# Performance work log

Measured on AMD Instinct MI355X. Metric: run time of the kernel, lower is better.

## Reference

```python
import jax, jax.numpy as jnp
import numpy as np

BN_EPS = 1e-5
TAU = 1.0  # gumbel temperature

def setup_inputs() -> dict:
    key = jax.random.key(0)
    ks = jax.random.split(key, 6)
    B, O, F, H, HID = 32, 4096, 256, 8, 128
    x = jax.random.normal(ks[0], (B, O, F), dtype=jnp.float32)
    gumbel_noise = jax.random.gumbel(ks[1], (B, O, H), dtype=jnp.float32)
    W_in = jax.random.normal(ks[2], (F, HID), dtype=jnp.float32) * (1.0 / np.sqrt(F))
    b_in = jnp.zeros((HID,), jnp.float32)
    W_blk = jax.random.normal(ks[3], (HID, HID), dtype=jnp.float32) * (1.0 / np.sqrt(HID))
    b_blk = jnp.zeros((HID,), jnp.float32)
    bn_gamma = jnp.ones((HID,), jnp.float32)
    bn_beta = jnp.zeros((HID,), jnp.float32)
    W_fc = jax.random.normal(ks[4], (HID, H), dtype=jnp.float32) * (1.0 / np.sqrt(HID))
    b_fc = jnp.zeros((H,), jnp.float32)
    return {"x": x, "gumbel_noise": gumbel_noise, "W_in": W_in, "b_in": b_in,
            "W_blk": W_blk, "b_blk": b_blk, "bn_gamma": bn_gamma, "bn_beta": bn_beta,
            "W_fc": W_fc, "b_fc": b_fc}

def reference(x, gumbel_noise, W_in, b_in, W_blk, b_blk, bn_gamma, bn_beta, W_fc, b_fc):
    B, O, F = x.shape
    xf = x.reshape(B * O, F)
    # DynamicNetwork head: input linear + relu, one residual block (Linear+BN+ReLU), fc
    h = jax.nn.relu(xf @ W_in + b_in)  # (B*O, HID)
    z = h @ W_blk + b_blk
    mu = z.mean(axis=0)
    var = z.var(axis=0)  # biased var, matches BatchNorm training normalization
    z = (z - mu) * jax.lax.rsqrt(var + BN_EPS) * bn_gamma + bn_beta
    h = jax.nn.relu(z) + h  # residual
    logits = (h @ W_fc + b_fc).reshape(B, O, -1)  # (B, O, H)
    # mask out zero-norm observations
    mask = (jnp.linalg.norm(x, axis=2) != 0)[..., None].astype(x.dtype)  # (B, O, 1)
    logits = logits * mask
    # gumbel softmax over observation dim (soft)
    w = jax.nn.softmax((logits + gumbel_noise) / TAU, axis=1)  # (B, O, H)
    # weighted sum pooling: algebraically the repeat-multiply-sum in the original
    pooled = jnp.einsum('boh,bof->bhf', w, x)  # (B, H, F)
    return pooled.reshape(B, -1)  # (B, H*F)
```

## Files before the change

kernel.cpp:

```cpp
#include <hip/hip_runtime.h>
#include <hip/hip_bf16.h>
#include <math.h>

#define MB_ 131072
#define F_  256
#define HID_ 128
#define H_  8
#define O_  4096
#define B_  32

typedef __attribute__((ext_vector_type(8))) short short8;
typedef __attribute__((ext_vector_type(4))) float f32x4;

static __device__ __forceinline__ unsigned short f2bf(float f) {
    unsigned int u = __float_as_uint(f);
    unsigned int r = (u + 0x7fffu + ((u >> 16) & 1u)) >> 16;
    return (unsigned short)r;
}
static __device__ __forceinline__ float bf2f(unsigned short u) {
    return __uint_as_float(((unsigned int)u) << 16);
}
static __device__ __forceinline__ float bflo(unsigned int u) {
    return __uint_as_float(u << 16);
}
static __device__ __forceinline__ float bfhi(unsigned int u) {
    return __uint_as_float(u & 0xffff0000u);
}

__global__ __launch_bounds__(256) void k_prep(
    const float* __restrict__ W_in, const float* __restrict__ W_blk,
    unsigned short* __restrict__ WinT, unsigned short* __restrict__ WblkT)
{
    const int idx = blockIdx.x * 256 + threadIdx.x;
    if (idx < 32768) {
        const int n = idx >> 8, k = idx & 255;
        WinT[idx] = f2bf(W_in[(size_t)k * HID_ + n]);
    } else {
        const int i2 = idx - 32768;
        const int n = i2 >> 7, k = i2 & 127;
        WblkT[i2] = f2bf(W_blk[(size_t)k * HID_ + n]);
    }
}

__global__ __launch_bounds__(256) void k_mfma_in(
    const float* __restrict__ x, const unsigned short* __restrict__ WinT,
    const float* __restrict__ b_in,
    unsigned short* __restrict__ h_out, float* __restrict__ mask_out)
{
    __shared__ unsigned short a_s[128 * 40];
    __shared__ unsigned short b_s[128 * 40];
    __shared__ float msum_s[128];
    const int tid = threadIdx.x;
    const int R0 = blockIdx.x * 128;
    const int lp_r = tid >> 3;
    const int lp_c = tid & 7;
    const int wave = tid >> 6;
    const int wrow = wave >> 1, wcol = wave & 1;
    const int lane = tid & 63;
    const int lm = lane & 15, quad = lane >> 4;

    if (tid < 128) msum_s[tid] = 0.f;
    float ms[4] = {0.f, 0.f, 0.f, 0.f};

    f32x4 acc[4][4];
#pragma unroll
    for (int i = 0; i < 4; i++)
#pragma unroll
        for (int j = 0; j < 4; j++) acc[i][j] = (f32x4){0.f, 0.f, 0.f, 0.f};

    for (int kt = 0; kt < 8; kt++) {
#pragma unroll
        for (int p = 0; p < 4; p++) {
            const int r = lp_r + 32 * p;
            const float4 v = *(const float4*)(x + (size_t)(R0 + r) * F_ + kt * 32 + lp_c * 4);
            ms[p] += v.x * v.x + v.y * v.y + v.z * v.z + v.w * v.w;
            ushort4 o;
            o.x = f2bf(v.x); o.y = f2bf(v.y); o.z = f2bf(v.z); o.w = f2bf(v.w);
            *(ushort4*)(&a_s[r * 40 + lp_c * 4]) = o;
        }
#pragma unroll
        for (int p = 0; p < 4; p++) {
            const int n = lp_r + 32 * p;
            const ushort4 wv = *(const ushort4*)(WinT + (size_t)n * F_ + kt * 32 + lp_c * 4);
            *(ushort4*)(&b_s[n * 40 + lp_c * 4]) = wv;
        }
        __syncthreads();
        short8 af[4], bfr[4];
#pragma unroll
        for (int mi = 0; mi < 4; mi++)
            af[mi] = *(const short8*)(&a_s[(wrow * 64 + mi * 16 + lm) * 40 + quad * 8]);
#pragma unroll
        for (int ni = 0; ni < 4; ni++)
            bfr[ni] = *(const short8*)(&b_s[(wcol * 64 + ni * 16 + lm) * 40 + quad * 8]);
#pragma unroll
        for (int mi = 0; mi < 4; mi++)
#pragma unroll
            for (int ni = 0; ni < 4; ni++)
                acc[mi][ni] = __builtin_amdgcn_mfma_f32_16x16x32_bf16(af[mi], bfr[ni], acc[mi][ni], 0, 0, 0);
        __syncthreads();
    }

#pragma unroll
    for (int p = 0; p < 4; p++) atomicAdd(&msum_s[lp_r + 32 * p], ms[p]);

    float bcol[4];
#pragma unroll
    for (int ni = 0; ni < 4; ni++) bcol[ni] = b_in[wcol * 64 + ni * 16 + lm];
#pragma unroll
    for (int mi = 0; mi < 4; mi++)
#pragma unroll
        for (int r = 0; r < 4; r++) {
            const size_t row = (size_t)R0 + wrow * 64 + mi * 16 + quad * 4 + r;
#pragma unroll
            for (int ni = 0; ni < 4; ni++) {
                const float v = fmaxf(acc[mi][ni][r] + bcol[ni], 0.f);
                h_out[row * HID_ + wcol * 64 + ni * 16 + lm] = f2bf(v);
            }
        }
    __syncthreads();
    if (tid < 128) mask_out[R0 + tid] = (msum_s[tid] != 0.f) ? 1.f : 0.f;
}

__global__ __launch_bounds__(256) void k_mfma_blk(
    const unsigned short* __restrict__ h_in, const unsigned short* __restrict__ WblkT,
    const float* __restrict__ b_blk, unsigned short* __restrict__ z_out,
    float* __restrict__ sumP, float* __restrict__ sumsqP)
{
    __shared__ unsigned short a_s[128 * 40];
    __shared__ unsigned short b_s[128 * 40];
    __shared__ float csum_s[128], csumsq_s[128];
    const int tid = threadIdx.x;
    const int R0 = blockIdx.x * 128;
    const int lp_r = tid >> 3;
    const int lp_c = tid & 7;
    const int wave = tid >> 6;
    const int wrow = wave >> 1, wcol = wave & 1;
    const int lane = tid & 63;
    const int lm = lane & 15, quad = lane >> 4;

    if (tid < 128) { csum_s[tid] = 0.f; csumsq_s[tid] = 0.f; }

    f32x4 acc[4][4];
#pragma unroll
    for (int i = 0; i < 4; i++)
#pragma unroll
        for (int j = 0; j < 4; j++) acc[i][j] = (f32x4){0.f, 0.f, 0.f, 0.f};

    for (int kt = 0; kt < 4; kt++) {
#pragma unroll
        for (int p = 0; p < 4; p++) {
            const int r = lp_r + 32 * p;
            const ushort4 v = *(const ushort4*)(h_in + (size_t)(R0 + r) * HID_ + kt * 32 + lp_c * 4);
            *(ushort4*)(&a_s[r * 40 + lp_c * 4]) = v;
        }
#pragma unroll
        for (int p = 0; p < 4; p++) {
            const int n = lp_r + 32 * p;
            const ushort4 wv = *(const ushort4*)(WblkT + (size_t)n * HID_ + kt * 32 + lp_c * 4);
            *(ushort4*)(&b_s[n * 40 + lp_c * 4]) = wv;
        }
        __syncthreads();
        short8 af[4], bfr[4];
#pragma unroll
        for (int mi = 0; mi < 4; mi++)
            af[mi] = *(const short8*)(&a_s[(wrow * 64 + mi * 16 + lm) * 40 + quad * 8]);
#pragma unroll
        for (int ni = 0; ni < 4; ni++)
            bfr[ni] = *(const short8*)(&b_s[(wcol * 64 + ni * 16 + lm) * 40 + quad * 8]);
#pragma unroll
        for (int mi = 0; mi < 4; mi++)
#pragma unroll
            for (int ni = 0; ni < 4; ni++)
                acc[mi][ni] = __builtin_amdgcn_mfma_f32_16x16x32_bf16(af[mi], bfr[ni], acc[mi][ni], 0, 0, 0);
        __syncthreads();
    }

    float bcol[4];
#pragma unroll
    for (int ni = 0; ni < 4; ni++) bcol[ni] = b_blk[wcol * 64 + ni * 16 + lm];
    float s_c[4] = {0.f, 0.f, 0.f, 0.f}, ss_c[4] = {0.f, 0.f, 0.f, 0.f};
#pragma unroll
    for (int mi = 0; mi < 4; mi++)
#pragma unroll
        for (int r = 0; r < 4; r++) {
            const size_t row = (size_t)R0 + wrow * 64 + mi * 16 + quad * 4 + r;
#pragma unroll
            for (int ni = 0; ni < 4; ni++) {
                const float zv = acc[mi][ni][r] + bcol[ni];
                s_c[ni] += zv;
                ss_c[ni] += zv * zv;
                z_out[row * HID_ + wcol * 64 + ni * 16 + lm] = f2bf(zv);
            }
        }
#pragma unroll
    for (int ni = 0; ni < 4; ni++) {
        atomicAdd(&csum_s[wcol * 64 + ni * 16 + lm], s_c[ni]);
        atomicAdd(&csumsq_s[wcol * 64 + ni * 16 + lm], ss_c[ni]);
    }
    __syncthreads();
    if (tid < 128) {
        sumP[(size_t)blockIdx.x * 128 + tid] = csum_s[tid];
        sumsqP[(size_t)blockIdx.x * 128 + tid] = csumsq_s[tid];
    }
}

__global__ __launch_bounds__(256) void k_bnfin(
    const float* __restrict__ sumP, const float* __restrict__ sumsqP,
    const float* __restrict__ gamma, const float* __restrict__ beta,
    float* __restrict__ scale, float* __restrict__ shift)
{
    const int c = blockIdx.x;
    const int tid = threadIdx.x;
    float s = 0.f, ss = 0.f;
    for (int i = tid; i < 1024; i += 256) {
        s  += sumP[(size_t)i * 128 + c];
        ss += sumsqP[(size_t)i * 128 + c];
    }
#pragma unroll
    for (int off = 32; off; off >>= 1) {
        s  += __shfl_xor(s, off, 64);
        ss += __shfl_xor(ss, off, 64);
    }
    __shared__ float rs[4], rss[4];
    const int wid = tid >> 6, lane = tid & 63;
    if (lane == 0) { rs[wid] = s; rss[wid] = ss; }
    __syncthreads();
    if (tid == 0) {
        const float S  = rs[0] + rs[1] + rs[2] + rs[3];
        const float SS = rss[0] + rss[1] + rss[2] + rss[3];
        const float inv_m = 1.0f / (float)MB_;
        const float mu = S * inv_m;
        const float var = SS * inv_m - mu * mu;
        const float sc = gamma[c] * rsqrtf(var + 1e-5f);
        scale[c] = sc;
        shift[c] = beta[c] - mu * sc;
    }
}

__global__ __launch_bounds__(256) void k_logits(
    const unsigned short* __restrict__ h_in, const unsigned short* __restrict__ z_in,
    const float* __restrict__ scale, const float* __restrict__ shift,
    const float* __restrict__ W_fc, const float* __restrict__ b_fc,
    const float* __restrict__ mask, const float* __restrict__ gumbel,
    float* __restrict__ t_out)
{
    __shared__ float wfc_s[128 * 8];
    __shared__ float sc_s[128], sh_s[128];
    const int tid = threadIdx.x;
    for (int i = tid; i < 1024; i += 256) wfc_s[i] = W_fc[i];
    if (tid < 128) { sc_s[tid] = scale[tid]; sh_s[tid] = shift[tid]; }
    __syncthreads();

    const size_t row = (size_t)blockIdx.x * 256 + tid;
    float acc[8];
#pragma unroll
    for (int j = 0; j < 8; j++) acc[j] = 0.f;

    const uint4* hp = (const uint4*)(h_in + row * HID_);
    const uint4* zp = (const uint4*)(z_in + row * HID_);
#pragma unroll 2
    for (int kc = 0; kc < 16; kc++) {
        const uint4 hq = hp[kc];
        const uint4 zq = zp[kc];
        unsigned int hs[4] = {hq.x, hq.y, hq.z, hq.w};
        unsigned int zs[4] = {zq.x, zq.y, zq.z, zq.w};
#pragma unroll
        for (int p = 0; p < 4; p++) {
            const int k = kc * 8 + p * 2;
            const float hf0 = bflo(hs[p]), hf1 = bfhi(hs[p]);
            const float zf0 = bflo(zs[p]), zf1 = bfhi(zs[p]);
            const float hb0 = fmaxf(zf0 * sc_s[k] + sh_s[k], 0.f) + hf0;
            const float hb1 = fmaxf(zf1 * sc_s[k + 1] + sh_s[k + 1], 0.f) + hf1;
#pragma unroll
            for (int j = 0; j < 8; j++)
                acc[j] += hb0 * wfc_s[k * 8 + j] + hb1 * wfc_s[(k + 1) * 8 + j];
        }
    }
    const float mk = mask[row];
    const float4 g0 = *(const float4*)(gumbel + row * 8);
    const float4 g1 = *(const float4*)(gumbel + row * 8 + 4);
    float4 t0, t1;
    t0.x = (acc[0] + b_fc[0]) * mk + g0.x;
    t0.y = (acc[1] + b_fc[1]) * mk + g0.y;
    t0.z = (acc[2] + b_fc[2]) * mk + g0.z;
    t0.w = (acc[3] + b_fc[3]) * mk + g0.w;
    t1.x = (acc[4] + b_fc[4]) * mk + g1.x;
    t1.y = (acc[5] + b_fc[5]) * mk + g1.y;
    t1.z = (acc[6] + b_fc[6]) * mk + g1.z;
    t1.w = (acc[7] + b_fc[7]) * mk + g1.w;
    *(float4*)(t_out + row * 8) = t0;
    *(float4*)(t_out + row * 8 + 4) = t1;
}

__global__ __launch_bounds__(256) void k_softmax(
    const float* __restrict__ t_in, float* __restrict__ w_out)
{
    const int bh = blockIdx.x;
    const int b = bh >> 3, hh = bh & 7;
    const int tid = threadIdx.x;
    const float* tp = t_in + (size_t)b * O_ * H_ + hh;
    float v[16];
    float mx = -3.4e38f;
#pragma unroll
    for (int it = 0; it < 16; it++) {
        v[it] = tp[(size_t)(it * 256 + tid) * 8];
        mx = fmaxf(mx, v[it]);
    }
#pragma unroll
    for (int off = 32; off; off >>= 1) mx = fmaxf(mx, __shfl_xor(mx, off, 64));
    __shared__ float rm[4];
    __shared__ float rsum[4];
    const int wid = tid >> 6, lane = tid & 63;
    if (lane == 0) rm[wid] = mx;
    __syncthreads();
    mx = fmaxf(fmaxf(rm[0], rm[1]), fmaxf(rm[2], rm[3]));
    float sum = 0.f;
#pragma unroll
    for (int it = 0; it < 16; it++) { v[it] = __expf(v[it] - mx); sum += v[it]; }
#pragma unroll
    for (int off = 32; off; off >>= 1) sum += __shfl_xor(sum, off, 64);
    if (lane == 0) rsum[wid] = sum;
    __syncthreads();
    sum = rsum[0] + rsum[1] + rsum[2] + rsum[3];
    const float inv = 1.f / sum;
    float* wp = w_out + (size_t)bh * O_;
#pragma unroll
    for (int it = 0; it < 16; it++) wp[it * 256 + tid] = v[it] * inv;
}

__global__ __launch_bounds__(256) void k_pool(
    const float* __restrict__ x, const float* __restrict__ w_in,
    float* __restrict__ pp)
{
    __shared__ float ws_s[8][256];
    const int tid = threadIdx.x;
    const int oc = blockIdx.x;
    const int b = blockIdx.y;
#pragma unroll
    for (int hh = 0; hh < 8; hh++)
        ws_s[hh][tid] = w_in[((size_t)(b * 8 + hh)) * O_ + oc * 256 + tid];
    __syncthreads();
    float acc[8];
#pragma unroll
    for (int hh = 0; hh < 8; hh++) acc[hh] = 0.f;
    const float* xp = x + ((size_t)b * O_ + oc * 256) * F_ + tid;
    for (int o = 0; o < 256; o++) {
        const float xv = xp[(size_t)o * F_];
#pragma unroll
        for (int hh = 0; hh < 8; hh++) acc[hh] += ws_s[hh][o] * xv;
    }
    float* outp = pp + ((size_t)oc * 32 + b) * 2048;
#pragma unroll
    for (int hh = 0; hh < 8; hh++) outp[hh * 256 + tid] = acc[hh];
}

__global__ __launch_bounds__(256) void k_reduce_pool(
    const float* __restrict__ pp, float* __restrict__ out)
{
    const size_t i = (size_t)blockIdx.x * 256 + threadIdx.x;
    float s = 0.f;
#pragma unroll
    for (int oc = 0; oc < 16; oc++) s += pp[(size_t)oc * 65536 + i];
    out[i] = s;
}

extern "C" void kernel_launch(void* const* d_in, const int* in_sizes, int n_in,
                              void* d_out, int out_size, void* d_ws, size_t ws_size,
                              hipStream_t stream)
{
    const float* x      = (const float*)d_in[0];
    const float* gumbel = (const float*)d_in[1];
    const float* W_in   = (const float*)d_in[2];
    const float* b_in   = (const float*)d_in[3];
    const float* W_blk  = (const float*)d_in[4];
    const float* b_blk  = (const float*)d_in[5];
    const float* gamma  = (const float*)d_in[6];
    const float* beta   = (const float*)d_in[7];
    const float* W_fc   = (const float*)d_in[8];
    const float* b_fc   = (const float*)d_in[9];
    float* out = (float*)d_out;
    char* ws = (char*)d_ws;

    unsigned short* h_bf  = (unsigned short*)(ws + 0);
    unsigned short* z_bf  = (unsigned short*)(ws + 33554432);
    float* mask   = (float*)(ws + 67108864);
    float* sumP   = (float*)(ws + 67633152);
    float* sumsqP = (float*)(ws + 68157440);
    float* scale  = (float*)(ws + 68681728);
    float* shift  = (float*)(ws + 68682240);
    float* t_buf  = (float*)(ws + 68682752);
    float* w_buf  = (float*)(ws + 72877056);
    float* pp     = (float*)(ws + 77071360);
    unsigned short* WinT  = (unsigned short*)(ws + 81265664);
    unsigned short* WblkT = (unsigned short*)(ws + 81331200);

    k_prep<<<192, 256, 0, stream>>>(W_in, W_blk, WinT, WblkT);
    k_mfma_in<<<1024, 256, 0, stream>>>(x, WinT, b_in, h_bf, mask);
    k_mfma_blk<<<1024, 256, 0, stream>>>(h_bf, WblkT, b_blk, z_bf, sumP, sumsqP);
    k_bnfin<<<128, 256, 0, stream>>>(sumP, sumsqP, gamma, beta, scale, shift);
    k_logits<<<512, 256, 0, stream>>>(h_bf, z_bf, scale, shift, W_fc, b_fc, mask, gumbel, t_buf);
    k_softmax<<<256, 256, 0, stream>>>(t_buf, w_buf);
    k_pool<<<dim3(16, 32), 256, 0, stream>>>(x, w_buf, pp);
    k_reduce_pool<<<256, 256, 0, stream>>>(pp, out);
}
```

Baseline: 303.5 us.

## Fuse both GEMMs into phase A, recompute z in logits kernel, transpose logits layout

The input GEMM and the block GEMM are merged into one kernel. h stays in shared memory and only BN statistics are produced, so z is never written to memory. The logits kernel recomputes z with MFMA from h instead of reading a stored z, then applies BN, the residual and fc, and writes logits in (b,h,o) layout so softmax can use contiguous float4 loads. The pooling kernel is split into twice as many O-chunks. This trades extra recompute of the second GEMM and a larger partial reduction for removing the 32MB z round trip.

```diff
diff --git a/kernel.cpp b/kernel.cpp
--- a/kernel.cpp
+++ b/kernel.cpp
@@ -19,12 +19,6 @@
 }
 static __device__ __forceinline__ float bf2f(unsigned short u) {
     return __uint_as_float(((unsigned int)u) << 16);
-}
-static __device__ __forceinline__ float bflo(unsigned int u) {
-    return __uint_as_float(u << 16);
-}
-static __device__ __forceinline__ float bfhi(unsigned int u) {
-    return __uint_as_float(u & 0xffff0000u);
 }
 
 __global__ __launch_bounds__(256) void k_prep(
@@ -42,14 +36,19 @@
     }
 }
 
-__global__ __launch_bounds__(256) void k_mfma_in(
+__global__ __launch_bounds__(256) void k_phaseA(
     const float* __restrict__ x, const unsigned short* __restrict__ WinT,
-    const float* __restrict__ b_in,
-    unsigned short* __restrict__ h_out, float* __restrict__ mask_out)
+    const unsigned short* __restrict__ WblkT,
+    const float* __restrict__ b_in, const float* __restrict__ b_blk,
+    unsigned short* __restrict__ h_out, float* __restrict__ mask_out,
+    float* __restrict__ sumP, float* __restrict__ sumsqP)
 {
     __shared__ unsigned short a_s[128 * 40];
     __shared__ unsigned short b_s[128 * 40];
+    __shared__ unsigned short hb_s[128 * 136];
     __shared__ float msum_s[128];
+    __shared__ float csum_s[128], csumsq_s[128];
+
     const int tid = threadIdx.x;
     const int R0 = blockIdx.x * 128;
     const int lp_r = tid >> 3;
@@ -59,7 +58,7 @@
     const int lane = tid & 63;
     const int lm = lane & 15, quad = lane >> 4;
 
-    if (tid < 128) msum_s[tid] = 0.f;
+    if (tid < 128) { msum_s[tid] = 0.f; csum_s[tid] = 0.f; csumsq_s[tid] = 0.f; }
     float ms[4] = {0.f, 0.f, 0.f, 0.f};
 
     f32x4 acc[4][4];
@@ -102,57 +101,39 @@
 
 #pragma unroll
     for (int p = 0; p < 4; p++) atomicAdd(&msum_s[lp_r + 32 * p], ms[p]);
-
-    float bcol[4];
-#pragma unroll
-    for (int ni = 0; ni < 4; ni++) bcol[ni] = b_in[wcol * 64 + ni * 16 + lm];
-#pragma unroll
-    for (int mi = 0; mi < 4; mi++)
-#pragma unroll
-        for (int r = 0; r < 4; r++) {
-            const size_t row = (size_t)R0 + wrow * 64 + mi * 16 + quad * 4 + r;
-#pragma unroll
-            for (int ni = 0; ni < 4; ni++) {
-                const float v = fmaxf(acc[mi][ni][r] + bcol[ni], 0.f);
-                h_out[row * HID_ + wcol * 64 + ni * 16 + lm] = f2bf(v);
+    {
+        float bcol[4];
+#pragma unroll
+        for (int ni = 0; ni < 4; ni++) bcol[ni] = b_in[wcol * 64 + ni * 16 + lm];
+#pragma unroll
+        for (int mi = 0; mi < 4; mi++)
+#pragma unroll
+            for (int r = 0; r < 4; r++) {
+                const int row = wrow * 64 + mi * 16 + quad * 4 + r;
+#pragma unroll
+                for (int ni = 0; ni < 4; ni++) {
+                    const int col = wcol * 64 + ni * 16 + lm;
+                    hb_s[row * 136 + col] = f2bf(fmaxf(acc[mi][ni][r] + bcol[ni], 0.f));
+                }
             }
-        }
-    __syncthreads();
+    }
+    __syncthreads();
+
+    {
+        const int row = tid >> 1, half = tid & 1;
+#pragma unroll
+        for (int c8 = 0; c8 < 8; c8++) {
+            const short8 v = *(const short8*)(&hb_s[row * 136 + half * 64 + c8 * 8]);
+            *(short8*)(h_out + (size_t)(R0 + row) * HID_ + half * 64 + c8 * 8) = v;
+        }
+    }
     if (tid < 128) mask_out[R0 + tid] = (msum_s[tid] != 0.f) ? 1.f : 0.f;
-}
-
-__global__ __launch_bounds__(256) void k_mfma_blk(
-    const unsigned short* __restrict__ h_in, const unsigned short* __restrict__ WblkT,
-    const float* __restrict__ b_blk, unsigned short* __restrict__ z_out,
-    float* __restrict__ sumP, float* __restrict__ sumsqP)
-{
-    __shared__ unsigned short a_s[128 * 40];
-    __shared__ unsigned short b_s[128 * 40];
-    __shared__ float csum_s[128], csumsq_s[128];
-    const int tid = threadIdx.x;
-    const int R0 = blockIdx.x * 128;
-    const int lp_r = tid >> 3;
-    const int lp_c = tid & 7;
-    const int wave = tid >> 6;
-    const int wrow = wave >> 1, wcol = wave & 1;
-    const int lane = tid & 63;
-    const int lm = lane & 15, quad = lane >> 4;
-
-    if (tid < 128) { csum_s[tid] = 0.f; csumsq_s[tid] = 0.f; }
-
-    f32x4 acc[4][4];
+
 #pragma unroll
     for (int i = 0; i < 4; i++)
 #pragma unroll
         for (int j = 0; j < 4; j++) acc[i][j] = (f32x4){0.f, 0.f, 0.f, 0.f};
-
     for (int kt = 0; kt < 4; kt++) {
-#pragma unroll
-        for (int p = 0; p < 4; p++) {
-            const int r = lp_r + 32 * p;
-            const ushort4 v = *(const ushort4*)(h_in + (size_t)(R0 + r) * HID_ + kt * 32 + lp_c * 4);
-            *(ushort4*)(&a_s[r * 40 + lp_c * 4]) = v;
-        }
 #pragma unroll
         for (int p = 0; p < 4; p++) {
             const int n = lp_r + 32 * p;
@@ -163,7 +144,7 @@
         short8 af[4], bfr[4];
 #pragma unroll
         for (int mi = 0; mi < 4; mi++)
-            af[mi] = *(const short8*)(&a_s[(wrow * 64 + mi * 16 + lm) * 40 + quad * 8]);
+            af[mi] = *(const short8*)(&hb_s[(wrow * 64 + mi * 16 + lm) * 136 + kt * 32 + quad * 8]);
 #pragma unroll
         for (int ni = 0; ni < 4; ni++)
             bfr[ni] = *(const short8*)(&b_s[(wcol * 64 + ni * 16 + lm) * 40 + quad * 8]);
@@ -175,27 +156,26 @@
         __syncthreads();
     }
 
-    float bcol[4];
-#pragma unroll
-    for (int ni = 0; ni < 4; ni++) bcol[ni] = b_blk[wcol * 64 + ni * 16 + lm];
-    float s_c[4] = {0.f, 0.f, 0.f, 0.f}, ss_c[4] = {0.f, 0.f, 0.f, 0.f};
-#pragma unroll
-    for (int mi = 0; mi < 4; mi++)
-#pragma unroll
-        for (int r = 0; r < 4; r++) {
-            const size_t row = (size_t)R0 + wrow * 64 + mi * 16 + quad * 4 + r;
-#pragma unroll
-            for (int ni = 0; ni < 4; ni++) {
-                const float zv = acc[mi][ni][r] + bcol[ni];
-                s_c[ni] += zv;
-                ss_c[ni] += zv * zv;
-                z_out[row * HID_ + wcol * 64 + ni * 16 + lm] = f2bf(zv);
-            }
-        }
-#pragma unroll
-    for (int ni = 0; ni < 4; ni++) {
-        atomicAdd(&csum_s[wcol * 64 + ni * 16 + lm], s_c[ni]);
-        atomicAdd(&csumsq_s[wcol * 64 + ni * 16 + lm], ss_c[ni]);
+    {
+        float bcol[4];
+#pragma unroll
+        for (int ni = 0; ni < 4; ni++) bcol[ni] = b_blk[wcol * 64 + ni * 16 + lm];
+        float s_c[4] = {0.f, 0.f, 0.f, 0.f}, ss_c[4] = {0.f, 0.f, 0.f, 0.f};
+#pragma unroll
+        for (int mi = 0; mi < 4; mi++)
+#pragma unroll
+            for (int r = 0; r < 4; r++)
+#pragma unroll
+                for (int ni = 0; ni < 4; ni++) {
+                    const float zv = acc[mi][ni][r] + bcol[ni];
+                    s_c[ni] += zv;
+                    ss_c[ni] += zv * zv;
+                }
+#pragma unroll
+        for (int ni = 0; ni < 4; ni++) {
+            atomicAdd(&csum_s[wcol * 64 + ni * 16 + lm], s_c[ni]);
+            atomicAdd(&csumsq_s[wcol * 64 + ni * 16 + lm], ss_c[ni]);
+        }
     }
     __syncthreads();
     if (tid < 128) {
@@ -237,86 +217,143 @@
     }
 }
 
-__global__ __launch_bounds__(256) void k_logits(
-    const unsigned short* __restrict__ h_in, const unsigned short* __restrict__ z_in,
+__global__ __launch_bounds__(256) void k_phaseC(
+    const unsigned short* __restrict__ h_in, const unsigned short* __restrict__ WblkT,
+    const float* __restrict__ b_blk,
     const float* __restrict__ scale, const float* __restrict__ shift,
     const float* __restrict__ W_fc, const float* __restrict__ b_fc,
     const float* __restrict__ mask, const float* __restrict__ gumbel,
-    float* __restrict__ t_out)
-{
+    float* __restrict__ t_bho)
+{
+    __shared__ unsigned short hb_s[128 * 136];
+    __shared__ unsigned short b_s[128 * 40];
     __shared__ float wfc_s[128 * 8];
     __shared__ float sc_s[128], sh_s[128];
+
     const int tid = threadIdx.x;
+    const int R0 = blockIdx.x * 128;
+    const int wave = tid >> 6;
+    const int wrow = wave >> 1, wcol = wave & 1;
+    const int lane = tid & 63;
+    const int lm = lane & 15, quad = lane >> 4;
+    const int lp_r = tid >> 3, lp_c = tid & 7;
+
     for (int i = tid; i < 1024; i += 256) wfc_s[i] = W_fc[i];
     if (tid < 128) { sc_s[tid] = scale[tid]; sh_s[tid] = shift[tid]; }
-    __syncthreads();
-
-    const size_t row = (size_t)blockIdx.x * 256 + tid;
-    float acc[8];
-#pragma unroll
-    for (int j = 0; j < 8; j++) acc[j] = 0.f;
-
-    const uint4* hp = (const uint4*)(h_in + row * HID_);
-    const uint4* zp = (const uint4*)(z_in + row * HID_);
-#pragma unroll 2
-    for (int kc = 0; kc < 16; kc++) {
-        const uint4 hq = hp[kc];
-        const uint4 zq = zp[kc];
-        unsigned int hs[4] = {hq.x, hq.y, hq.z, hq.w};
-        unsigned int zs[4] = {zq.x, zq.y, zq.z, zq.w};
+    {
+        const int row = tid >> 1, half = tid & 1;
+#pragma unroll
+        for (int c8 = 0; c8 < 8; c8++) {
+            const short8 v = *(const short8*)(h_in + (size_t)(R0 + row) * HID_ + half * 64 + c8 * 8);
+            *(short8*)(&hb_s[row * 136 + half * 64 + c8 * 8]) = v;
+        }
+    }
+    __syncthreads();
+
+    f32x4 acc[4][4];
+#pragma unroll
+    for (int i = 0; i < 4; i++)
+#pragma unroll
+        for (int j = 0; j < 4; j++) acc[i][j] = (f32x4){0.f, 0.f, 0.f, 0.f};
+    for (int kt = 0; kt < 4; kt++) {
 #pragma unroll
         for (int p = 0; p < 4; p++) {
-            const int k = kc * 8 + p * 2;
-            const float hf0 = bflo(hs[p]), hf1 = bfhi(hs[p]);
-            const float zf0 = bflo(zs[p]), zf1 = bfhi(zs[p]);
-            const float hb0 = fmaxf(zf0 * sc_s[k] + sh_s[k], 0.f) + hf0;
-            const float hb1 = fmaxf(zf1 * sc_s[k + 1] + sh_s[k + 1], 0.f) + hf1;
-#pragma unroll
-            for (int j = 0; j < 8; j++)
-                acc[j] += hb0 * wfc_s[k * 8 + j] + hb1 * wfc_s[(k + 1) * 8 + j];
-        }
-    }
-    const float mk = mask[row];
-    const float4 g0 = *(const float4*)(gumbel + row * 8);
-    const float4 g1 = *(const float4*)(gumbel + row * 8 + 4);
-    float4 t0, t1;
-    t0.x = (acc[0] + b_fc[0]) * mk + g0.x;
-    t0.y = (acc[1] + b_fc[1]) * mk + g0.y;
-    t0.z = (acc[2] + b_fc[2]) * mk + g0.z;
-    t0.w = (acc[3] + b_fc[3]) * mk + g0.w;
-    t1.x = (acc[4] + b_fc[4]) * mk + g1.x;
-    t1.y = (acc[5] + b_fc[5]) * mk + g1.y;
-    t1.z = (acc[6] + b_fc[6]) * mk + g1.z;
-    t1.w = (acc[7] + b_fc[7]) * mk + g1.w;
-    *(float4*)(t_out + row * 8) = t0;
-    *(float4*)(t_out + row * 8 + 4) = t1;
+            const int n = lp_r + 32 * p;
+            const ushort4 wv = *(const ushort4*)(WblkT + (size_t)n * HID_ + kt * 32 + lp_c * 4);
+            *(ushort4*)(&b_s[n * 40 + lp_c * 4]) = wv;
+        }
+        __syncthreads();
+        short8 af[4], bfr[4];
+#pragma unroll
+        for (int mi = 0; mi < 4; mi++)
+            af[mi] = *(const short8*)(&hb_s[(wrow * 64 + mi * 16 + lm) * 136 + kt * 32 + quad * 8]);
+#pragma unroll
+        for (int ni = 0; ni < 4; ni++)
+            bfr[ni] = *(const short8*)(&b_s[(wcol * 64 + ni * 16 + lm) * 40 + quad * 8]);
+#pragma unroll
+        for (int mi = 0; mi < 4; mi++)
+#pragma unroll
+            for (int ni = 0; ni < 4; ni++)
+                acc[mi][ni] = __builtin_amdgcn_mfma_f32_16x16x32_bf16(af[mi], bfr[ni], acc[mi][ni], 0, 0, 0);
+        __syncthreads();
+    }
+
+    {
+        float bcol[4];
+#pragma unroll
+        for (int ni = 0; ni < 4; ni++) bcol[ni] = b_blk[wcol * 64 + ni * 16 + lm];
+#pragma unroll
+        for (int mi = 0; mi < 4; mi++)
+#pragma unroll
+            for (int r = 0; r < 4; r++) {
+                const int row = wrow * 64 + mi * 16 + quad * 4 + r;
+#pragma unroll
+                for (int ni = 0; ni < 4; ni++) {
+                    const int col = wcol * 64 + ni * 16 + lm;
+                    const float zv = acc[mi][ni][r] + bcol[ni];
+                    const float hv = bf2f(hb_s[row * 136 + col]);
+                    const float hb = fmaxf(zv * sc_s[col] + sh_s[col], 0.f) + hv;
+                    hb_s[row * 136 + col] = f2bf(hb);
+                }
+            }
+    }
+    __syncthreads();
+
+    if (tid < 128) {
+        const int row = tid;
+        const int grow = R0 + row;
+        const int b = grow >> 12, o = grow & 4095;
+        float a8[8];
+#pragma unroll
+        for (int j = 0; j < 8; j++) a8[j] = 0.f;
+#pragma unroll 4
+        for (int k8 = 0; k8 < 16; k8++) {
+            const short8 hv8 = *(const short8*)(&hb_s[row * 136 + k8 * 8]);
+#pragma unroll
+            for (int e = 0; e < 8; e++) {
+                const float hv = bf2f((unsigned short)hv8[e]);
+                const int k = k8 * 8 + e;
+#pragma unroll
+                for (int j = 0; j < 8; j++) a8[j] += hv * wfc_s[k * 8 + j];
+            }
+        }
+        const float mk = mask[grow];
+        const float* gp = gumbel + (size_t)grow * 8;
+#pragma unroll
+        for (int j = 0; j < 8; j++) {
+            const float t = (a8[j] + b_fc[j]) * mk + gp[j];
+            t_bho[((size_t)(b * 8 + j)) * O_ + o] = t;
+        }
+    }
 }
 
 __global__ __launch_bounds__(256) void k_softmax(
     const float* __restrict__ t_in, float* __restrict__ w_out)
 {
     const int bh = blockIdx.x;
-    const int b = bh >> 3, hh = bh & 7;
     const int tid = threadIdx.x;
-    const float* tp = t_in + (size_t)b * O_ * H_ + hh;
-    float v[16];
+    const float* tp = t_in + (size_t)bh * O_;
+    float4 v[4];
     float mx = -3.4e38f;
 #pragma unroll
-    for (int it = 0; it < 16; it++) {
-        v[it] = tp[(size_t)(it * 256 + tid) * 8];
-        mx = fmaxf(mx, v[it]);
+    for (int it = 0; it < 4; it++) {
+        v[it] = *(const float4*)(tp + it * 1024 + tid * 4);
+        mx = fmaxf(mx, fmaxf(fmaxf(v[it].x, v[it].y), fmaxf(v[it].z, v[it].w)));
     }
 #pragma unroll
     for (int off = 32; off; off >>= 1) mx = fmaxf(mx, __shfl_xor(mx, off, 64));
-    __shared__ float rm[4];
-    __shared__ float rsum[4];
+    __shared__ float rm[4], rsum[4];
     const int wid = tid >> 6, lane = tid & 63;
     if (lane == 0) rm[wid] = mx;
     __syncthreads();
     mx = fmaxf(fmaxf(rm[0], rm[1]), fmaxf(rm[2], rm[3]));
     float sum = 0.f;
 #pragma unroll
-    for (int it = 0; it < 16; it++) { v[it] = __expf(v[it] - mx); sum += v[it]; }
+    for (int it = 0; it < 4; it++) {
+        v[it].x = __expf(v[it].x - mx); v[it].y = __expf(v[it].y - mx);
+        v[it].z = __expf(v[it].z - mx); v[it].w = __expf(v[it].w - mx);
+        sum += v[it].x + v[it].y + v[it].z + v[it].w;
+    }
 #pragma unroll
     for (int off = 32; off; off >>= 1) sum += __shfl_xor(sum, off, 64);
     if (lane == 0) rsum[wid] = sum;
@@ -325,33 +362,45 @@
     const float inv = 1.f / sum;
     float* wp = w_out + (size_t)bh * O_;
 #pragma unroll
-    for (int it = 0; it < 16; it++) wp[it * 256 + tid] = v[it] * inv;
+    for (int it = 0; it < 4; it++) {
+        float4 o;
+        o.x = v[it].x * inv; o.y = v[it].y * inv; o.z = v[it].z * inv; o.w = v[it].w * inv;
+        *(float4*)(wp + it * 1024 + tid * 4) = o;
+    }
 }
 
 __global__ __launch_bounds__(256) void k_pool(
     const float* __restrict__ x, const float* __restrict__ w_in,
     float* __restrict__ pp)
 {
-    __shared__ float ws_s[8][256];
+    __shared__ float ws_s[8][128];
     const int tid = threadIdx.x;
     const int oc = blockIdx.x;
     const int b = blockIdx.y;
-#pragma unroll
-    for (int hh = 0; hh < 8; hh++)
-        ws_s[hh][tid] = w_in[((size_t)(b * 8 + hh)) * O_ + oc * 256 + tid];
+    const int wave = tid >> 6, lane = tid & 63;
+    const int f = wave * 64 + lane;
+    for (int i = tid; i < 1024; i += 256) {
+        const int hh = i >> 7, oi = i & 127;
+        ws_s[hh][oi] = w_in[((size_t)(b * 8 + hh)) * O_ + oc * 128 + oi];
+    }
     __syncthreads();
     float acc[8];
 #pragma unroll
     for (int hh = 0; hh < 8; hh++) acc[hh] = 0.f;
-    const float* xp = x + ((size_t)b * O_ + oc * 256) * F_ + tid;
-    for (int o = 0; o < 256; o++) {
-        const float xv = xp[(size_t)o * F_];
-#pragma unroll
-        for (int hh = 0; hh < 8; hh++) acc[hh] += ws_s[hh][o] * xv;
-    }
-    float* outp = pp + ((size_t)oc * 32 + b) * 2048;
-#pragma unroll
-    for (int hh = 0; hh < 8; hh++) outp[hh * 256 + tid] = acc[hh];
+    const float* xp = x + ((size_t)(b * O_ + oc * 128)) * F_ + f;
+#pragma unroll 1
+    for (int oi = 0; oi < 128; oi += 4) {
+        float xv[4];
+#pragma unroll
+        for (int u = 0; u < 4; u++) xv[u] = xp[(size_t)(oi + u) * F_];
+#pragma unroll
+        for (int u = 0; u < 4; u++)
+#pragma unroll
+            for (int hh = 0; hh < 8; hh++) acc[hh] += ws_s[hh][oi + u] * xv[u];
+    }
+    float* outp = pp + ((size_t)(oc * 32 + b)) * 2048;
+#pragma unroll
+    for (int hh = 0; hh < 8; hh++) outp[hh * 256 + f] = acc[hh];
 }
 
 __global__ __launch_bounds__(256) void k_reduce_pool(
@@ -360,7 +409,7 @@
     const size_t i = (size_t)blockIdx.x * 256 + threadIdx.x;
     float s = 0.f;
 #pragma unroll
-    for (int oc = 0; oc < 16; oc++) s += pp[(size_t)oc * 65536 + i];
+    for (int oc = 0; oc < 32; oc++) s += pp[(size_t)oc * 65536 + i];
     out[i] = s;
 }
 
@@ -382,24 +431,22 @@
     char* ws = (char*)d_ws;
 
     unsigned short* h_bf  = (unsigned short*)(ws + 0);
-    unsigned short* z_bf  = (unsigned short*)(ws + 33554432);
-    float* mask   = (float*)(ws + 67108864);
-    float* sumP   = (float*)(ws + 67633152);
-    float* sumsqP = (float*)(ws + 68157440);
-    float* scale  = (float*)(ws + 68681728);
-    float* shift  = (float*)(ws + 68682240);
-    float* t_buf  = (float*)(ws + 68682752);
-    float* w_buf  = (float*)(ws + 72877056);
-    float* pp     = (float*)(ws + 77071360);
-    unsigned short* WinT  = (unsigned short*)(ws + 81265664);
-    unsigned short* WblkT = (unsigned short*)(ws + 81331200);
+    float* mask   = (float*)(ws + 33554432);
+    float* sumP   = (float*)(ws + 34078720);
+    float* sumsqP = (float*)(ws + 34603008);
+    float* scale  = (float*)(ws + 35127296);
+    float* shift  = (float*)(ws + 35127808);
+    float* t_buf  = (float*)(ws + 35128320);
+    float* w_buf  = (float*)(ws + 39322624);
+    float* pp     = (float*)(ws + 43516928);
+    unsigned short* WinT  = (unsigned short*)(ws + 51905536);
+    unsigned short* WblkT = (unsigned short*)(ws + 51971072);
 
     k_prep<<<192, 256, 0, stream>>>(W_in, W_blk, WinT, WblkT);
-    k_mfma_in<<<1024, 256, 0, stream>>>(x, WinT, b_in, h_bf, mask);
-    k_mfma_blk<<<1024, 256, 0, stream>>>(h_bf, WblkT, b_blk, z_bf, sumP, sumsqP);
+    k_phaseA<<<1024, 256, 0, stream>>>(x, WinT, WblkT, b_in, b_blk, h_bf, mask, sumP, sumsqP);
     k_bnfin<<<128, 256, 0, stream>>>(sumP, sumsqP, gamma, beta, scale, shift);
-    k_logits<<<512, 256, 0, stream>>>(h_bf, z_bf, scale, shift, W_fc, b_fc, mask, gumbel, t_buf);
+    k_phaseC<<<1024, 256, 0, stream>>>(h_bf, WblkT, b_blk, scale, shift, W_fc, b_fc, mask, gumbel, t_buf);
     k_softmax<<<256, 256, 0, stream>>>(t_buf, w_buf);
-    k_pool<<<dim3(16, 32), 256, 0, stream>>>(x, w_buf, pp);
+    k_pool<<<dim3(32, 32), 256, 0, stream>>>(x, w_buf, pp);
     k_reduce_pool<<<256, 256, 0, stream>>>(pp, out);
 }
```

Result: slower. 318.4 us (+4.9%).
